# Optimization experiments

Hardware: AMD Instinct MI355X
Metric: run time of the kernel (lower is better)

Reference implementation:

```python
import jax, jax.numpy as jnp
import numpy as np

N_NODES = 10000
N_EDGES = 160000
MUL = 128            # channel multiplicity
N_SPECIES = 4        # node_attrs scalars
N_RADIAL = 8         # edge_feats scalars
AVG_NEIGH = 16.0
SQRT3 = 1.7320508075688772


def setup_inputs() -> dict:
    key = jax.random.key(0)
    ks = jax.random.split(key, 16)
    inp = {}
    inp['node_attrs'] = jax.random.uniform(ks[0], (N_NODES, N_SPECIES), dtype=jnp.float32)
    inp['node_feats'] = jax.random.normal(ks[1], (N_NODES, MUL * 4), dtype=jnp.float32)  # 128x0e + 128x1o
    inp['edge_attrs'] = jax.random.normal(ks[2], (N_EDGES, 4), dtype=jnp.float32)        # 1x0e + 1x1o (SH lmax=1)
    inp['edge_feats'] = jax.random.normal(ks[3], (N_EDGES, N_RADIAL), dtype=jnp.float32)
    inp['edge_index'] = jax.random.randint(ks[4], (2, N_EDGES), 0, N_NODES, dtype=jnp.int32)
    # linear_up: per-l mixing (o3.Linear on 128x0e+128x1o)
    inp['W_up0'] = jax.random.normal(ks[5], (MUL, MUL), dtype=jnp.float32)
    inp['W_up1'] = jax.random.normal(ks[6], (MUL, MUL), dtype=jnp.float32)
    # radial MLP [8, 64, 64, 512] (conv_tp.weight_numel = 4 instructions * 128)
    inp['W_mlp1'] = jax.random.normal(ks[7], (N_RADIAL, 64), dtype=jnp.float32)
    inp['W_mlp2'] = jax.random.normal(ks[8], (64, 64), dtype=jnp.float32)
    inp['W_mlp3'] = jax.random.normal(ks[9], (64, 4 * MUL), dtype=jnp.float32)
    # linear: irreps_mid.simplify() = 256x0e + 256x1o -> 128x0e + 128x1o
    inp['W_lin0'] = jax.random.normal(ks[10], (2 * MUL, MUL), dtype=jnp.float32)
    inp['W_lin1'] = jax.random.normal(ks[11], (2 * MUL, MUL), dtype=jnp.float32)
    # skip_tp: FullyConnectedTensorProduct(target, 4x0e -> target), uvw weights per l
    inp['W_skip0'] = jax.random.normal(ks[12], (MUL, N_SPECIES, MUL), dtype=jnp.float32)
    inp['W_skip1'] = jax.random.normal(ks[13], (MUL, N_SPECIES, MUL), dtype=jnp.float32)
    inp['update_coeff_param'] = jnp.zeros((1,), dtype=jnp.float32)
    return inp


def reference(node_attrs, node_feats, edge_attrs, edge_feats, edge_index,
              W_up0, W_up1, W_mlp1, W_mlp2, W_mlp3, W_lin0, W_lin1,
              W_skip0, W_skip1, update_coeff_param):
    N = node_feats.shape[0]
    # split node feats into irrep blocks: scalars [N,128], vectors [N,128,3]
    s = node_feats[:, :MUL]
    v = node_feats[:, MUL:].reshape(N, MUL, 3)
    # linear_up (o3.Linear, fan-in normalized)
    inv_up = 1.0 / jnp.sqrt(jnp.float32(MUL))
    s = (s @ W_up0) * inv_up
    v = jnp.einsum('nui,uw->nwi', v, W_up1) * inv_up
    # radial MLP -> per-edge TP weights (e3nn FullyConnectedNet style, fan-in normalized, silu)
    h = jax.nn.silu((edge_feats @ W_mlp1) / jnp.sqrt(jnp.float32(N_RADIAL)))
    h = jax.nn.silu((h @ W_mlp2) / jnp.sqrt(jnp.float32(64)))
    tpw = (h @ W_mlp3) / jnp.sqrt(jnp.float32(64))  # [E, 512]
    # instruction order (sorted by output irrep): 0e*0e->0e, 1o*1o->0e, 0e*1o->1o, 1o*0e->1o
    w_a, w_b, w_c, w_d = tpw[:, :MUL], tpw[:, MUL:2*MUL], tpw[:, 2*MUL:3*MUL], tpw[:, 3*MUL:]
    sender, receiver = edge_index[0], edge_index[1]
    xs = s[sender]          # [E,128] gather
    xv = v[sender]          # [E,128,3]
    ea_s = edge_attrs[:, :1]    # [E,1]
    ea_v = edge_attrs[:, 1:4]   # [E,3]
    # CG tensor-product messages ('uvu', component norm)
    m0 = w_a * xs * ea_s                                        # 0e x 0e -> 0e
    m1 = w_b * (jnp.einsum('eui,ei->eu', xv, ea_v) / SQRT3)      # 1o x 1o -> 0e
    m2 = (w_c * xs)[:, :, None] * ea_v[:, None, :]               # 0e x 1o -> 1o
    m3 = w_d[:, :, None] * xv * ea_s[:, :, None]                 # 1o x 0e -> 1o
    ms = jnp.concatenate([m0, m1], axis=1)                       # [E,256]
    mv = jnp.concatenate([m2, m3], axis=1)                       # [E,256,3]
    # scatter-sum to receiver nodes
    Ms = jax.ops.segment_sum(ms, receiver, num_segments=N)       # [N,256]
    Mv = jax.ops.segment_sum(mv, receiver, num_segments=N)       # [N,256,3]
    # linear (256x0e+256x1o -> 128x0e+128x1o), divided by avg_num_neighbors
    inv_lin = 1.0 / (jnp.sqrt(jnp.float32(2 * MUL)) * AVG_NEIGH)
    S = (Ms @ W_lin0) * inv_lin                                  # [N,128]
    V = jnp.einsum('nui,uw->nwi', Mv, W_lin1) * inv_lin          # [N,128,3]
    # skip_tp: FullyConnectedTensorProduct(message, node_attrs) with uvw weights
    inv_sk = 1.0 / jnp.sqrt(jnp.float32(MUL * N_SPECIES))
    sc_s = jnp.einsum('nu,nv,uvw->nw', S, node_attrs, W_skip0) * inv_sk
    sc_v = jnp.einsum('nui,nv,uvw->nwi', V, node_attrs, W_skip1) * inv_sk
    # residual stream mixing (sc=False branch)
    c = jax.nn.sigmoid(update_coeff_param)                       # [1]
    c_old = jax.lax.rsqrt(c * c + 1.0)
    c_new = c * c_old
    S = c_old * S + c_new * sc_s
    V = c_old * V + c_new * sc_v
    # reshape_irreps: [N, mul, 1 + 3]
    out = jnp.concatenate([S[:, :, None], V], axis=-1)           # [N,128,4]
    return out
```

## Files before the change

kernel.cpp:

```cpp
#include <hip/hip_runtime.h>

#define MUL 128

typedef __attribute__((ext_vector_type(8))) short bf16x8;
typedef __attribute__((ext_vector_type(4))) short bf16x4;
typedef __attribute__((ext_vector_type(4))) float f32x4;

__device__ __constant__ float kINV_UP   = 0.08838834764831845f;
__device__ __constant__ float kINV_L1   = 0.35355339059327373f;
__device__ __constant__ float kINV_L2   = 0.125f;
__device__ __constant__ float kINV_L3   = 0.125f;
__device__ __constant__ float kINV_LIN  = 0.00390625f;
__device__ __constant__ float kINV_SK   = 0.044194173824159216f;
__device__ __constant__ float kINV_SQ3  = 0.5773502691896258f;

#define WAVE_LDS_SYNC() asm volatile("s_waitcnt lgkmcnt(0)" ::: "memory")

static __device__ __forceinline__ short f2bf(float f) {
  unsigned u = __float_as_uint(f);
  unsigned r = (u + 0x7FFFu + ((u >> 16) & 1u)) >> 16;
  return (short)r;
}

__global__ __launch_bounds__(256) void k_cvtcnt(
    const float* __restrict__ W_up0, const float* __restrict__ W_up1,
    const float* __restrict__ W_lin0, const float* __restrict__ W_lin1,
    const float* __restrict__ W_sk0, const float* __restrict__ W_sk1,
    const float* __restrict__ W_mlp2, const float* __restrict__ W_mlp3,
    short* __restrict__ W0T, short* __restrict__ W1T,
    short* __restrict__ Wl0T, short* __restrict__ Wl1T,
    short* __restrict__ Wsk0T, short* __restrict__ Wsk1T,
    short* __restrict__ W2T, short* __restrict__ W3T,
    const int* __restrict__ eidx, int* __restrict__ cnt, int E, int CVT_B) {
  int blk = blockIdx.x;
  if (blk >= CVT_B) {
    int e = (blk - CVT_B) * 256 + threadIdx.x;
    if (e < E) atomicAdd(&cnt[eidx[E + e]], 1);
    return;
  }
  int id = blk * 256 + threadIdx.x;
  if (id < 16384) {
    int w = id >> 7, u = id & 127;
    W0T[id] = f2bf(W_up0[u * 128 + w]);
    return;
  }
  id -= 16384;
  if (id < 16384) {
    int w = id >> 7, u = id & 127;
    W1T[id] = f2bf(W_up1[u * 128 + w]);
    return;
  }
  id -= 16384;
  if (id < 32768) {
    int w = id >> 8, u = id & 255;
    Wl0T[id] = f2bf(W_lin0[u * 128 + w]);
    return;
  }
  id -= 32768;
  if (id < 32768) {
    int w = id >> 8, u = id & 255;
    Wl1T[id] = f2bf(W_lin1[u * 128 + w]);
    return;
  }
  id -= 32768;
  if (id < 65536) {
    int w = id >> 9, k = id & 511;
    int v = k >> 7, u = k & 127;
    Wsk0T[id] = f2bf(W_sk0[(u * 4 + v) * 128 + w]);
    return;
  }
  id -= 65536;
  if (id < 65536) {
    int w = id >> 9, k = id & 511;
    int v = k >> 7, u = k & 127;
    Wsk1T[id] = f2bf(W_sk1[(u * 4 + v) * 128 + w]);
    return;
  }
  id -= 65536;
  if (id < 4096) {
    int c = id >> 6, k = id & 63;
    W2T[id] = f2bf(W_mlp2[k * 64 + c]);
    return;
  }
  id -= 4096;
  if (id < 32768) {
    int c = id >> 6, k = id & 63;
    W3T[id] = f2bf(W_mlp3[k * 512 + c]);
  }
}

__global__ __launch_bounds__(1024) void k_scan(const int* __restrict__ cnt,
                                               int* __restrict__ offs,
                                               int* __restrict__ cursor, int N) {
  __shared__ int part[1024];
  const int t = threadIdx.x;
  int CH = (N + 1023) >> 10;
  if (CH > 16) CH = 16;
  const int base = t * CH;
  int loc[16];
  int s = 0;
  for (int i = 0; i < CH; ++i) {
    int idx = base + i;
    loc[i] = (idx < N) ? cnt[idx] : 0;
    s += loc[i];
  }
  part[t] = s;
  __syncthreads();
  for (int off = 1; off < 1024; off <<= 1) {
    int v = part[t];
    int add = (t >= off) ? part[t - off] : 0;
    __syncthreads();
    part[t] = v + add;
    __syncthreads();
  }
  int excl = part[t] - s;
  for (int i = 0; i < CH; ++i) {
    int idx = base + i;
    if (idx < N) { offs[idx] = excl; cursor[idx] = excl; }
    excl += loc[i];
  }
  if (t == 1023) offs[N] = part[1023];
}

__global__ __launch_bounds__(256) void k_fused3(
    const int* __restrict__ eidx, int* __restrict__ cursor, int* __restrict__ sorted,
    const float* __restrict__ nf, const short* __restrict__ W0T,
    const short* __restrict__ W1T, float* __restrict__ s_up, float* __restrict__ v_up,
    const float* __restrict__ ef, const float* __restrict__ W1f,
    const short* __restrict__ W2T, const short* __restrict__ W3T,
    unsigned* __restrict__ tpw2, int N, int E, int MLP_B, int UP_B) {
  __shared__ __align__(16) char smem[29696];
  const int t = threadIdx.x;
  int blk = blockIdx.x;

  if (blk < MLP_B) {
    float* sW1  = (float*)smem;
    short* sW2T = (short*)(smem + 2048);
    short* sh1  = (short*)(smem + 11264);
    short* sh2  = (short*)(smem + 20480);

    for (int i = t * 4; i < 512; i += 1024)
      *reinterpret_cast<float4*>(&sW1[i]) = *reinterpret_cast<const float4*>(W1f + i);
    for (int i = t * 8; i < 4096; i += 2048) {
      int r = i >> 6, c = i & 63;
      *reinterpret_cast<bf16x8*>(&sW2T[r * 72 + c]) =
          *reinterpret_cast<const bf16x8*>(&W2T[r * 64 + c]);
    }
    __syncthreads();

    const int w = t >> 6, l = t & 63, li = l & 15, g = l >> 4;
    const int e = blk * 64 + w * 16 + li;
    short* h1row = sh1 + (w * 16 + li) * 72;
    short* h2row = sh2 + (w * 16 + li) * 72;

    float4 qa = {0.f, 0.f, 0.f, 0.f}, qb = {0.f, 0.f, 0.f, 0.f};
    if (e < E) {
      qa = *reinterpret_cast<const float4*>(ef + (size_t)e * 8);
      qb = *reinterpret_cast<const float4*>(ef + (size_t)e * 8 + 4);
    }
    const float x[8] = {qa.x, qa.y, qa.z, qa.w, qb.x, qb.y, qb.z, qb.w};
    {
      bf16x8 p0, p1;
#pragma unroll
      for (int j = 0; j < 16; ++j) {
        int col = g * 16 + j;
        float a = 0.f;
#pragma unroll
        for (int k = 0; k < 8; ++k) a += x[k] * sW1[k * 64 + col];
        a *= kINV_L1;
        short hv = f2bf(a / (1.f + __expf(-a)));
        if (j < 8) p0[j] = hv; else p1[j - 8] = hv;
      }
      *reinterpret_cast<bf16x8*>(&h1row[g * 16])     = p0;
      *reinterpret_cast<bf16x8*>(&h1row[g * 16 + 8]) = p1;
    }
    WAVE_LDS_SYNC();

    {
      bf16x8 b0 = *reinterpret_cast<const bf16x8*>(&h1row[g * 8]);
      bf16x8 b1 = *reinterpret_cast<const bf16x8*>(&h1row[32 + g * 8]);
#pragma unroll
      for (int ct = 0; ct < 4; ++ct) {
        const short* wrow = &sW2T[(ct * 16 + li) * 72];
        bf16x8 a0 = *reinterpret_cast<const bf16x8*>(&wrow[g * 8]);
        bf16x8 a1 = *reinterpret_cast<const bf16x8*>(&wrow[32 + g * 8]);
        f32x4 acc = {0.f, 0.f, 0.f, 0.f};
        acc = __builtin_amdgcn_mfma_f32_16x16x32_bf16(a0, b0, acc, 0, 0, 0);
        acc = __builtin_amdgcn_mfma_f32_16x16x32_bf16(a1, b1, acc, 0, 0, 0);
        bf16x4 hq;
#pragma unroll
        for (int r = 0; r < 4; ++r) {
          float a = acc[r] * kINV_L2;
          hq[r] = f2bf(a / (1.f + __expf(-a)));
        }
        *reinterpret_cast<bf16x4*>(&h2row[ct * 16 + g * 4]) = hq;
      }
    }
    WAVE_LDS_SYNC();

    {
      bf16x8 b0 = *reinterpret_cast<const bf16x8*>(&h2row[g * 8]);
      bf16x8 b1 = *reinterpret_cast<const bf16x8*>(&h2row[32 + g * 8]);
#pragma unroll 4
      for (int rt = 0; rt < 16; ++rt) {
        const int rowA = rt * 16 + li;
        bf16x8 a0 = *reinterpret_cast<const bf16x8*>(&W3T[(size_t)rowA * 64 + g * 8]);
        bf16x8 a1 = *reinterpret_cast<const bf16x8*>(&W3T[(size_t)rowA * 64 + 32 + g * 8]);
        bf16x8 a2 = *reinterpret_cast<const bf16x8*>(&W3T[(size_t)(rowA + 256) * 64 + g * 8]);
        bf16x8 a3 = *reinterpret_cast<const bf16x8*>(&W3T[(size_t)(rowA + 256) * 64 + 32 + g * 8]);
        f32x4 accA = {0.f, 0.f, 0.f, 0.f};
        f32x4 accB = {0.f, 0.f, 0.f, 0.f};
        accA = __builtin_amdgcn_mfma_f32_16x16x32_bf16(a0, b0, accA, 0, 0, 0);
        accA = __builtin_amdgcn_mfma_f32_16x16x32_bf16(a1, b1, accA, 0, 0, 0);
        accB = __builtin_amdgcn_mfma_f32_16x16x32_bf16(a2, b0, accB, 0, 0, 0);
        accB = __builtin_amdgcn_mfma_f32_16x16x32_bf16(a3, b1, accB, 0, 0, 0);
        if (e < E) {
          uint4 d;
          unsigned* dp = &d.x;
#pragma unroll
          for (int r = 0; r < 4; ++r) {
            unsigned lo = (unsigned)(unsigned short)f2bf(accA[r] * kINV_L3);
            unsigned hi = (unsigned)(unsigned short)f2bf(accB[r] * kINV_L3);
            dp[r] = lo | (hi << 16);
          }
          *reinterpret_cast<uint4*>(&tpw2[(size_t)e * 256 + rt * 16 + g * 4]) = d;
        }
      }
    }
    return;
  }
  blk -= MLP_B;

  if (blk < UP_B) {
    short* lsA = (short*)smem;
    const int nb = blk * 16;

    for (int base = t * 8; base < 16 * 512; base += 256 * 8) {
      int n = base >> 9, j0 = base & 511;
      float vals[8];
      if (nb + n < N) {
        float4 q0 = *reinterpret_cast<const float4*>(nf + (size_t)(nb + n) * 512 + j0);
        float4 q1 = *reinterpret_cast<const float4*>(nf + (size_t)(nb + n) * 512 + j0 + 4);
        vals[0] = q0.x; vals[1] = q0.y; vals[2] = q0.z; vals[3] = q0.w;
        vals[4] = q1.x; vals[5] = q1.y; vals[6] = q1.z; vals[7] = q1.w;
      } else {
#pragma unroll
        for (int e = 0; e < 8; ++e) vals[e] = 0.f;
      }
#pragma unroll
      for (int e = 0; e < 8; ++e) {
        int idx = j0 + e;
        if (idx < 128) {
          lsA[(0 * 16 + n) * 136 + idx] = f2bf(vals[e]);
        } else {
          unsigned q = idx - 128;
          unsigned u = q / 3u;
          unsigned i = q - u * 3u;
          lsA[((1 + i) * 16 + n) * 136 + u] = f2bf(vals[e]);
        }
      }
    }
    __syncthreads();

    const int c = t >> 6;
    const int lane = t & 63;
    const int col = lane & 15;
    const int g = lane >> 4;

    const short* WT = c ? W1T : W0T;

    bf16x8 af[4];
#pragma unroll
    for (int kk = 0; kk < 4; ++kk)
      af[kk] = *reinterpret_cast<const bf16x8*>(&lsA[(c * 16 + col) * 136 + kk * 32 + g * 8]);

#pragma unroll
    for (int nt = 0; nt < 8; ++nt) {
      f32x4 acc = {0.f, 0.f, 0.f, 0.f};
#pragma unroll
      for (int kk = 0; kk < 4; ++kk) {
        bf16x8 bf = *reinterpret_cast<const bf16x8*>(&WT[(size_t)(nt * 16 + col) * 128 + kk * 32 + g * 8]);
        acc = __builtin_amdgcn_mfma_f32_16x16x32_bf16(af[kk], bf, acc, 0, 0, 0);
      }
#pragma unroll
      for (int r = 0; r < 4; ++r) {
        int nd = nb + g * 4 + r;
        if (nd < N) {
          float val = acc[r] * kINV_UP;
          if (c == 0) s_up[(size_t)nd * 128 + nt * 16 + col] = val;
          else        v_up[(size_t)nd * 384 + (c - 1) * 128 + nt * 16 + col] = val;
        }
      }
    }
    return;
  }
  blk -= UP_B;

  int e = blk * 256 + t;
  if (e < E) {
    int r = eidx[E + e];
    int p = atomicAdd(&cursor[r], 1);
    sorted[p] = e;
  }
}

__global__ __launch_bounds__(256) void k_gather(
    const int* __restrict__ sorted, const int* __restrict__ offs,
    const unsigned* __restrict__ tpw2, const float* __restrict__ eattr,
    const int* __restrict__ eidx,
    const float* __restrict__ s_up, const float* __restrict__ v_up,
    float* __restrict__ Ms, float* __restrict__ Mv, int N, int SB) {
  const int t = threadIdx.x;
  const int vside = blockIdx.x >= SB;
  const int nb = (vside ? blockIdx.x - SB : blockIdx.x) * 4;
  const int n = nb + (t >> 6);
  if (n >= N) return;
  const int l = t & 63;
  const int u0 = l * 2;

  float aMs0 = 0.f, aMs1 = 0.f;
  float aV[3][2] = {};

  const int e0 = offs[n], e1 = offs[n + 1];

  if (!vside) {
    for (int p = e0; p < e1; ++p) {
      int eid = sorted[p];
      int snd = eidx[eid];
      float4 ea = *reinterpret_cast<const float4*>(eattr + (size_t)eid * 4);
      uint2 q = *reinterpret_cast<const uint2*>(tpw2 + (size_t)eid * 256 + u0);
      float2 xs = *reinterpret_cast<const float2*>(s_up + (size_t)snd * 128 + u0);
      float tA0 = __uint_as_float(q.x << 16);
      float tB0 = __uint_as_float(q.x & 0xFFFF0000u);
      float tA1 = __uint_as_float(q.y << 16);
      float tB1 = __uint_as_float(q.y & 0xFFFF0000u);
      float xe0 = xs.x * ea.x, xe1 = xs.y * ea.x;
      aMs0 += tA0 * xe0;
      aMs1 += tA1 * xe1;
      float wc0 = tB0 * xs.x, wc1 = tB1 * xs.y;
      aV[0][0] += wc0 * ea.y; aV[0][1] += wc1 * ea.y;
      aV[1][0] += wc0 * ea.z; aV[1][1] += wc1 * ea.z;
      aV[2][0] += wc0 * ea.w; aV[2][1] += wc1 * ea.w;
    }
    *reinterpret_cast<float2*>(Ms + (size_t)n * 256 + u0) = make_float2(aMs0, aMs1);
#pragma unroll
    for (int i = 0; i < 3; ++i)
      *reinterpret_cast<float2*>(Mv + (size_t)n * 768 + i * 256 + u0) =
          make_float2(aV[i][0], aV[i][1]);
  } else {
    for (int p = e0; p < e1; ++p) {
      int eid = sorted[p];
      int snd = eidx[eid];
      float4 ea = *reinterpret_cast<const float4*>(eattr + (size_t)eid * 4);
      uint2 q = *reinterpret_cast<const uint2*>(tpw2 + (size_t)eid * 256 + 128 + u0);
      const float* xv = v_up + (size_t)snd * 384 + u0;
      float2 x0 = *reinterpret_cast<const float2*>(xv);
      float2 x1 = *reinterpret_cast<const float2*>(xv + 128);
      float2 x2 = *reinterpret_cast<const float2*>(xv + 256);
      float tA0 = __uint_as_float(q.x << 16);
      float tB0 = __uint_as_float(q.x & 0xFFFF0000u);
      float tA1 = __uint_as_float(q.y << 16);
      float tB1 = __uint_as_float(q.y & 0xFFFF0000u);
      float dot0 = x0.x * ea.y + x1.x * ea.z + x2.x * ea.w;
      float dot1 = x0.y * ea.y + x1.y * ea.z + x2.y * ea.w;
      aMs0 += tA0 * dot0 * kINV_SQ3;
      aMs1 += tA1 * dot1 * kINV_SQ3;
      float wd0 = tB0 * ea.x, wd1 = tB1 * ea.x;
      aV[0][0] += wd0 * x0.x; aV[0][1] += wd1 * x0.y;
      aV[1][0] += wd0 * x1.x; aV[1][1] += wd1 * x1.y;
      aV[2][0] += wd0 * x2.x; aV[2][1] += wd1 * x2.y;
    }
    *reinterpret_cast<float2*>(Ms + (size_t)n * 256 + 128 + u0) = make_float2(aMs0, aMs1);
#pragma unroll
    for (int i = 0; i < 3; ++i)
      *reinterpret_cast<float2*>(Mv + (size_t)n * 768 + i * 256 + 128 + u0) =
          make_float2(aV[i][0], aV[i][1]);
  }
}

__global__ __launch_bounds__(256) void k_linskip(
    const float* __restrict__ Ms, const float* __restrict__ Mv,
    const short* __restrict__ Wl0T, const short* __restrict__ Wl1T,
    const short* __restrict__ Wsk0T, const short* __restrict__ Wsk1T,
    const float* __restrict__ attrs, const float* __restrict__ upd,
    float* __restrict__ out, int N) {
  __shared__ __align__(16) short lsA[4][16][264];
  __shared__ __align__(16) short lsS[4][16][136];
  __shared__ float sat[16][4];
  const int nb = blockIdx.x * 16;
  const int t = threadIdx.x;

  for (int base = t * 4; base < 16 * 1024; base += 1024) {
    int n = base >> 10, j = base & 1023;
    int comp = j >> 8, u = j & 255;
    float4 q = {0.f, 0.f, 0.f, 0.f};
    if (nb + n < N) {
      const float* src = (comp == 0) ? (Ms + (size_t)(nb + n) * 256 + u)
                                     : (Mv + (size_t)(nb + n) * 768 + (size_t)(comp - 1) * 256 + u);
      q = *reinterpret_cast<const float4*>(src);
    }
    lsA[comp][n][u + 0] = f2bf(q.x);
    lsA[comp][n][u + 1] = f2bf(q.y);
    lsA[comp][n][u + 2] = f2bf(q.z);
    lsA[comp][n][u + 3] = f2bf(q.w);
  }
  if (t < 64) {
    int n = t >> 2, v = t & 3;
    sat[n][v] = (nb + n < N) ? attrs[(size_t)(nb + n) * 4 + v] : 0.f;
  }
  __syncthreads();

  const int c = t >> 6;
  const int lane = t & 63;
  const int col = lane & 15;
  const int g = lane >> 4;

  const short* WLT = c ? Wl1T : Wl0T;
  const short* WST = c ? Wsk1T : Wsk0T;

  bf16x8 af1[8];
#pragma unroll
  for (int kk = 0; kk < 8; ++kk)
    af1[kk] = *reinterpret_cast<const bf16x8*>(&lsA[c][col][kk * 32 + g * 8]);

  f32x4 Sreg[8];
#pragma unroll
  for (int nt = 0; nt < 8; ++nt) {
    f32x4 acc = {0.f, 0.f, 0.f, 0.f};
#pragma unroll
    for (int kk = 0; kk < 8; ++kk) {
      bf16x8 bf = *reinterpret_cast<const bf16x8*>(&WLT[(size_t)(nt * 16 + col) * 256 + kk * 32 + g * 8]);
      acc = __builtin_amdgcn_mfma_f32_16x16x32_bf16(af1[kk], bf, acc, 0, 0, 0);
    }
#pragma unroll
    for (int r = 0; r < 4; ++r) acc[r] *= kINV_LIN;
    Sreg[nt] = acc;
#pragma unroll
    for (int r = 0; r < 4; ++r)
      lsS[c][g * 4 + r][nt * 16 + col] = f2bf(acc[r]);
  }

  float satr[4][4];
#pragma unroll
  for (int r = 0; r < 4; ++r)
#pragma unroll
    for (int v = 0; v < 4; ++v) satr[r][v] = sat[g * 4 + r][v];

  __syncthreads();

  bf16x8 af2[4];
#pragma unroll
  for (int kk = 0; kk < 4; ++kk)
    af2[kk] = *reinterpret_cast<const bf16x8*>(&lsS[c][col][kk * 32 + g * 8]);

  const float p = upd[0];
  const float cc = 1.f / (1.f + __expf(-p));
  const float c_old = rsqrtf(cc * cc + 1.f);
  const float c_new = cc * c_old;

#pragma unroll
  for (int nt = 0; nt < 8; ++nt) {
    float fin[4] = {0.f, 0.f, 0.f, 0.f};
#pragma unroll
    for (int v = 0; v < 4; ++v) {
      f32x4 tmp = {0.f, 0.f, 0.f, 0.f};
#pragma unroll
      for (int kk = 0; kk < 4; ++kk) {
        bf16x8 bf = *reinterpret_cast<const bf16x8*>(&WST[(size_t)(nt * 16 + col) * 512 + v * 128 + kk * 32 + g * 8]);
        tmp = __builtin_amdgcn_mfma_f32_16x16x32_bf16(af2[kk], bf, tmp, 0, 0, 0);
      }
#pragma unroll
      for (int r = 0; r < 4; ++r) fin[r] += satr[r][v] * tmp[r];
    }
#pragma unroll
    for (int r = 0; r < 4; ++r) {
      int nd = nb + g * 4 + r;
      if (nd < N) {
        float val = c_old * Sreg[nt][r] + c_new * fin[r] * kINV_SK;
        out[((size_t)nd * 128 + nt * 16 + col) * 4 + c] = val;
      }
    }
  }
}

extern "C" void kernel_launch(void* const* d_in, const int* in_sizes, int n_in,
                              void* d_out, int out_size, void* d_ws, size_t ws_size,
                              hipStream_t stream) {
  const float* node_attrs = (const float*)d_in[0];
  const float* node_feats = (const float*)d_in[1];
  const float* edge_attrs = (const float*)d_in[2];
  const float* edge_feats = (const float*)d_in[3];
  const int*   edge_index = (const int*)d_in[4];
  const float* W_up0  = (const float*)d_in[5];
  const float* W_up1  = (const float*)d_in[6];
  const float* W_mlp1 = (const float*)d_in[7];
  const float* W_mlp2 = (const float*)d_in[8];
  const float* W_mlp3 = (const float*)d_in[9];
  const float* W_lin0 = (const float*)d_in[10];
  const float* W_lin1 = (const float*)d_in[11];
  const float* W_skip0 = (const float*)d_in[12];
  const float* W_skip1 = (const float*)d_in[13];
  const float* upd = (const float*)d_in[14];
  float* out = (float*)d_out;

  const int N = in_sizes[0] / 4;
  const int E = in_sizes[4] / 2;

  float* ws = (float*)d_ws;
  float* s_up = ws;
  float* v_up = s_up + (size_t)N * 128;
  float* Ms   = v_up + (size_t)N * 384;
  float* Mv   = Ms + (size_t)N * 256;
  int* cnt    = (int*)(Mv + (size_t)N * 768);
  int* offs   = cnt + N;
  int* cursor = offs + N + 1;
  int* sorted = cursor + N;

  short* wbase = (short*)((((uintptr_t)(sorted + E)) + 15) & ~(uintptr_t)15);
  short* W0T   = wbase;
  short* W1T   = W0T + 16384;
  short* Wl0T  = W1T + 16384;
  short* Wl1T  = Wl0T + 32768;
  short* Wsk0T = Wl1T + 32768;
  short* Wsk1T = Wsk0T + 65536;
  short* W2T   = Wsk1T + 65536;
  short* W3T   = W2T + 4096;
  unsigned* tpw2 = (unsigned*)(W3T + 32768);

  const int CVT_B = (266240 + 255) / 256;
  const int CNT_B = (E + 255) / 256;
  const int MLP_B = (E + 63) / 64;
  const int UP_B  = (N + 15) / 16;
  const int SC_B  = (E + 255) / 256;
  const int SB    = (N + 3) / 4;

  hipMemsetAsync(cnt, 0, (size_t)N * sizeof(int), stream);

  k_cvtcnt<<<CVT_B + CNT_B, 256, 0, stream>>>(
      W_up0, W_up1, W_lin0, W_lin1, W_skip0, W_skip1, W_mlp2, W_mlp3,
      W0T, W1T, Wl0T, Wl1T, Wsk0T, Wsk1T, W2T, W3T,
      edge_index, cnt, E, CVT_B);
  k_scan<<<1, 1024, 0, stream>>>(cnt, offs, cursor, N);
  k_fused3<<<MLP_B + UP_B + SC_B, 256, 0, stream>>>(
      edge_index, cursor, sorted,
      node_feats, W0T, W1T, s_up, v_up,
      edge_feats, W_mlp1, W2T, W3T, tpw2, N, E, MLP_B, UP_B);
  k_gather<<<2 * SB, 256, 0, stream>>>(sorted, offs, tpw2, edge_attrs, edge_index,
                                       s_up, v_up, Ms, Mv, N, SB);
  k_linskip<<<(N + 15) / 16, 256, 0, stream>>>(Ms, Mv, Wl0T, Wl1T, Wsk0T, Wsk1T,
                                               node_attrs, upd, out, N);
}
```

Before: 316.8 us.

## Process two edge tiles per wave in radial MLP and prefetch W3T rows

Each MLP block now handles 128 edges (two 16-edge tiles per wave), so every W2T/W3T fragment loaded is reused across two MFMA sets, halving weight loads per edge and halving the number of MLP blocks. The layer-3 loop also software-prefetches the next W3T row tile into registers before issuing the current MFMAs. The change raises LDS use to about 47 KB and increases register pressure, which may lower occupancy for all blocks of the fused kernel.

After: 282.2 us. -10.9%, faster.

```diff
diff --git a/kernel.cpp b/kernel.cpp
--- a/kernel.cpp
+++ b/kernel.cpp
@@ -129,7 +129,7 @@
     const float* __restrict__ ef, const float* __restrict__ W1f,
     const short* __restrict__ W2T, const short* __restrict__ W3T,
     unsigned* __restrict__ tpw2, int N, int E, int MLP_B, int UP_B) {
-  __shared__ __align__(16) char smem[29696];
+  __shared__ __align__(16) char smem[48128];
   const int t = threadIdx.x;
   int blk = blockIdx.x;
 
@@ -137,7 +137,7 @@
     float* sW1  = (float*)smem;
     short* sW2T = (short*)(smem + 2048);
     short* sh1  = (short*)(smem + 11264);
-    short* sh2  = (short*)(smem + 20480);
+    short* sh2  = (short*)(smem + 29696);
 
     for (int i = t * 4; i < 512; i += 1024)
       *reinterpret_cast<float4*>(&sW1[i]) = *reinterpret_cast<const float4*>(W1f + i);
@@ -149,82 +149,118 @@
     __syncthreads();
 
     const int w = t >> 6, l = t & 63, li = l & 15, g = l >> 4;
-    const int e = blk * 64 + w * 16 + li;
-    short* h1row = sh1 + (w * 16 + li) * 72;
-    short* h2row = sh2 + (w * 16 + li) * 72;
-
-    float4 qa = {0.f, 0.f, 0.f, 0.f}, qb = {0.f, 0.f, 0.f, 0.f};
-    if (e < E) {
-      qa = *reinterpret_cast<const float4*>(ef + (size_t)e * 8);
-      qb = *reinterpret_cast<const float4*>(ef + (size_t)e * 8 + 4);
-    }
-    const float x[8] = {qa.x, qa.y, qa.z, qa.w, qb.x, qb.y, qb.z, qb.w};
+    const int eb = blk * 128 + w * 32;
+    const int es0 = eb + li, es1 = eb + 16 + li;
+    short* h1r0 = sh1 + (w * 32 + li) * 72;
+    short* h1r1 = sh1 + (w * 32 + 16 + li) * 72;
+    short* h2r0 = sh2 + (w * 32 + li) * 72;
+    short* h2r1 = sh2 + (w * 32 + 16 + li) * 72;
+
     {
-      bf16x8 p0, p1;
-#pragma unroll
-      for (int j = 0; j < 16; ++j) {
-        int col = g * 16 + j;
-        float a = 0.f;
-#pragma unroll
-        for (int k = 0; k < 8; ++k) a += x[k] * sW1[k * 64 + col];
-        a *= kINV_L1;
-        short hv = f2bf(a / (1.f + __expf(-a)));
-        if (j < 8) p0[j] = hv; else p1[j - 8] = hv;
-      }
-      *reinterpret_cast<bf16x8*>(&h1row[g * 16])     = p0;
-      *reinterpret_cast<bf16x8*>(&h1row[g * 16 + 8]) = p1;
+#pragma unroll
+      for (int s = 0; s < 2; ++s) {
+        const int e = s ? es1 : es0;
+        short* h1row = s ? h1r1 : h1r0;
+        float4 qa = {0.f, 0.f, 0.f, 0.f}, qb = {0.f, 0.f, 0.f, 0.f};
+        if (e < E) {
+          qa = *reinterpret_cast<const float4*>(ef + (size_t)e * 8);
+          qb = *reinterpret_cast<const float4*>(ef + (size_t)e * 8 + 4);
+        }
+        const float x[8] = {qa.x, qa.y, qa.z, qa.w, qb.x, qb.y, qb.z, qb.w};
+        bf16x8 p0, p1;
+#pragma unroll
+        for (int j = 0; j < 16; ++j) {
+          int col = g * 16 + j;
+          float a = 0.f;
+#pragma unroll
+          for (int k = 0; k < 8; ++k) a += x[k] * sW1[k * 64 + col];
+          a *= kINV_L1;
+          short hv = f2bf(a / (1.f + __expf(-a)));
+          if (j < 8) p0[j] = hv; else p1[j - 8] = hv;
+        }
+        *reinterpret_cast<bf16x8*>(&h1row[g * 16])     = p0;
+        *reinterpret_cast<bf16x8*>(&h1row[g * 16 + 8]) = p1;
+      }
     }
     WAVE_LDS_SYNC();
 
     {
-      bf16x8 b0 = *reinterpret_cast<const bf16x8*>(&h1row[g * 8]);
-      bf16x8 b1 = *reinterpret_cast<const bf16x8*>(&h1row[32 + g * 8]);
+      bf16x8 hb0[2], hb1[2];
+      hb0[0] = *reinterpret_cast<const bf16x8*>(&h1r0[g * 8]);
+      hb1[0] = *reinterpret_cast<const bf16x8*>(&h1r0[32 + g * 8]);
+      hb0[1] = *reinterpret_cast<const bf16x8*>(&h1r1[g * 8]);
+      hb1[1] = *reinterpret_cast<const bf16x8*>(&h1r1[32 + g * 8]);
 #pragma unroll
       for (int ct = 0; ct < 4; ++ct) {
         const short* wrow = &sW2T[(ct * 16 + li) * 72];
         bf16x8 a0 = *reinterpret_cast<const bf16x8*>(&wrow[g * 8]);
         bf16x8 a1 = *reinterpret_cast<const bf16x8*>(&wrow[32 + g * 8]);
-        f32x4 acc = {0.f, 0.f, 0.f, 0.f};
-        acc = __builtin_amdgcn_mfma_f32_16x16x32_bf16(a0, b0, acc, 0, 0, 0);
-        acc = __builtin_amdgcn_mfma_f32_16x16x32_bf16(a1, b1, acc, 0, 0, 0);
-        bf16x4 hq;
-#pragma unroll
-        for (int r = 0; r < 4; ++r) {
-          float a = acc[r] * kINV_L2;
-          hq[r] = f2bf(a / (1.f + __expf(-a)));
-        }
-        *reinterpret_cast<bf16x4*>(&h2row[ct * 16 + g * 4]) = hq;
+#pragma unroll
+        for (int s = 0; s < 2; ++s) {
+          f32x4 acc = {0.f, 0.f, 0.f, 0.f};
+          acc = __builtin_amdgcn_mfma_f32_16x16x32_bf16(a0, hb0[s], acc, 0, 0, 0);
+          acc = __builtin_amdgcn_mfma_f32_16x16x32_bf16(a1, hb1[s], acc, 0, 0, 0);
+          bf16x4 hq;
+#pragma unroll
+          for (int r = 0; r < 4; ++r) {
+            float a = acc[r] * kINV_L2;
+            hq[r] = f2bf(a / (1.f + __expf(-a)));
+          }
+          *reinterpret_cast<bf16x4*>(&((s ? h2r1 : h2r0)[ct * 16 + g * 4])) = hq;
+        }
       }
     }
     WAVE_LDS_SYNC();
 
     {
-      bf16x8 b0 = *reinterpret_cast<const bf16x8*>(&h2row[g * 8]);
-      bf16x8 b1 = *reinterpret_cast<const bf16x8*>(&h2row[32 + g * 8]);
-#pragma unroll 4
+      bf16x8 b0[2], b1[2];
+      b0[0] = *reinterpret_cast<const bf16x8*>(&h2r0[g * 8]);
+      b1[0] = *reinterpret_cast<const bf16x8*>(&h2r0[32 + g * 8]);
+      b0[1] = *reinterpret_cast<const bf16x8*>(&h2r1[g * 8]);
+      b1[1] = *reinterpret_cast<const bf16x8*>(&h2r1[32 + g * 8]);
+      const bool ok0 = es0 < E, ok1 = es1 < E;
+
+      bf16x8 c0, c1, c2, c3;
+      {
+        const int rowA = li;
+        c0 = *reinterpret_cast<const bf16x8*>(&W3T[(size_t)rowA * 64 + g * 8]);
+        c1 = *reinterpret_cast<const bf16x8*>(&W3T[(size_t)rowA * 64 + 32 + g * 8]);
+        c2 = *reinterpret_cast<const bf16x8*>(&W3T[(size_t)(rowA + 256) * 64 + g * 8]);
+        c3 = *reinterpret_cast<const bf16x8*>(&W3T[(size_t)(rowA + 256) * 64 + 32 + g * 8]);
+      }
+#pragma unroll
       for (int rt = 0; rt < 16; ++rt) {
-        const int rowA = rt * 16 + li;
-        bf16x8 a0 = *reinterpret_cast<const bf16x8*>(&W3T[(size_t)rowA * 64 + g * 8]);
-        bf16x8 a1 = *reinterpret_cast<const bf16x8*>(&W3T[(size_t)rowA * 64 + 32 + g * 8]);
-        bf16x8 a2 = *reinterpret_cast<const bf16x8*>(&W3T[(size_t)(rowA + 256) * 64 + g * 8]);
-        bf16x8 a3 = *reinterpret_cast<const bf16x8*>(&W3T[(size_t)(rowA + 256) * 64 + 32 + g * 8]);
-        f32x4 accA = {0.f, 0.f, 0.f, 0.f};
-        f32x4 accB = {0.f, 0.f, 0.f, 0.f};
-        accA = __builtin_amdgcn_mfma_f32_16x16x32_bf16(a0, b0, accA, 0, 0, 0);
-        accA = __builtin_amdgcn_mfma_f32_16x16x32_bf16(a1, b1, accA, 0, 0, 0);
-        accB = __builtin_amdgcn_mfma_f32_16x16x32_bf16(a2, b0, accB, 0, 0, 0);
-        accB = __builtin_amdgcn_mfma_f32_16x16x32_bf16(a3, b1, accB, 0, 0, 0);
-        if (e < E) {
-          uint4 d;
-          unsigned* dp = &d.x;
-#pragma unroll
-          for (int r = 0; r < 4; ++r) {
-            unsigned lo = (unsigned)(unsigned short)f2bf(accA[r] * kINV_L3);
-            unsigned hi = (unsigned)(unsigned short)f2bf(accB[r] * kINV_L3);
-            dp[r] = lo | (hi << 16);
+        bf16x8 n0, n1, n2, n3;
+        const bool pf = (rt < 15);
+        if (pf) {
+          const int rowA = (rt + 1) * 16 + li;
+          n0 = *reinterpret_cast<const bf16x8*>(&W3T[(size_t)rowA * 64 + g * 8]);
+          n1 = *reinterpret_cast<const bf16x8*>(&W3T[(size_t)rowA * 64 + 32 + g * 8]);
+          n2 = *reinterpret_cast<const bf16x8*>(&W3T[(size_t)(rowA + 256) * 64 + g * 8]);
+          n3 = *reinterpret_cast<const bf16x8*>(&W3T[(size_t)(rowA + 256) * 64 + 32 + g * 8]);
+        }
+#pragma unroll
+        for (int s = 0; s < 2; ++s) {
+          f32x4 accA = {0.f, 0.f, 0.f, 0.f};
+          f32x4 accB = {0.f, 0.f, 0.f, 0.f};
+          accA = __builtin_amdgcn_mfma_f32_16x16x32_bf16(c0, b0[s], accA, 0, 0, 0);
+          accA = __builtin_amdgcn_mfma_f32_16x16x32_bf16(c1, b1[s], accA, 0, 0, 0);
+          accB = __builtin_amdgcn_mfma_f32_16x16x32_bf16(c2, b0[s], accB, 0, 0, 0);
+          accB = __builtin_amdgcn_mfma_f32_16x16x32_bf16(c3, b1[s], accB, 0, 0, 0);
+          if (s ? ok1 : ok0) {
+            uint4 d;
+            unsigned* dp = &d.x;
+#pragma unroll
+            for (int r = 0; r < 4; ++r) {
+              unsigned lo = (unsigned)(unsigned short)f2bf(accA[r] * kINV_L3);
+              unsigned hi = (unsigned)(unsigned short)f2bf(accB[r] * kINV_L3);
+              dp[r] = lo | (hi << 16);
+            }
+            *reinterpret_cast<uint4*>(
+                &tpw2[(size_t)(s ? es1 : es0) * 256 + rt * 16 + g * 4]) = d;
           }
-          *reinterpret_cast<uint4*>(&tpw2[(size_t)e * 256 + rt * 16 + g * 4]) = d;
-        }
+        }
+        if (pf) { c0 = n0; c1 = n1; c2 = n2; c3 = n3; }
       }
     }
     return;
@@ -529,7 +565,7 @@
 
   const int CVT_B = (266240 + 255) / 256;
   const int CNT_B = (E + 255) / 256;
-  const int MLP_B = (E + 63) / 64;
+  const int MLP_B = (E + 127) / 128;
   const int UP_B  = (N + 15) / 16;
   const int SC_B  = (E + 255) / 256;
   const int SB    = (N + 3) / 4;
```

## Fuse radial MLP into receiver-sorted message aggregation with segmented atomic adds

Applied to the files above, without the earlier changes.

Removes the separate radial-MLP pass that wrote per-edge bf16 tensor-product weights to global memory. Each block now takes 32 receiver-sorted edge records and computes the MLP for them, keeping the weights in LDS. It then accumulates messages per receiver run and flushes them with float atomics into Ms/Mv, which are zeroed by extra blocks in the first kernel. This cuts a large global write and read of per-edge weights, at the cost of atomics at block boundaries, non-deterministic summation order, and more LDS per block.

After: 371.2 us. +17.2%, slower.

```diff
diff --git a/kernel.cpp b/kernel.cpp
--- a/kernel.cpp
+++ b/kernel.cpp
@@ -14,12 +14,13 @@
 __device__ __constant__ float kINV_SK   = 0.044194173824159216f;
 __device__ __constant__ float kINV_SQ3  = 0.5773502691896258f;
 
-#define WAVE_LDS_SYNC() asm volatile("s_waitcnt lgkmcnt(0)" ::: "memory")
-
 static __device__ __forceinline__ short f2bf(float f) {
   unsigned u = __float_as_uint(f);
   unsigned r = (u + 0x7FFFu + ((u >> 16) & 1u)) >> 16;
   return (short)r;
+}
+static __device__ __forceinline__ float bf2f(short s) {
+  return __uint_as_float(((unsigned)(unsigned short)s) << 16);
 }
 
 __global__ __launch_bounds__(256) void k_cvtcnt(
@@ -31,8 +32,15 @@
     short* __restrict__ Wl0T, short* __restrict__ Wl1T,
     short* __restrict__ Wsk0T, short* __restrict__ Wsk1T,
     short* __restrict__ W2T, short* __restrict__ W3T,
-    const int* __restrict__ eidx, int* __restrict__ cnt, int E, int CVT_B) {
+    const int* __restrict__ eidx, int* __restrict__ cnt,
+    float* __restrict__ Mzero, int E, int CVT_B, int CNT_B) {
   int blk = blockIdx.x;
+  if (blk >= CVT_B + CNT_B) {
+    size_t off = (size_t)(blk - CVT_B - CNT_B) * 1024 + threadIdx.x * 4;
+    float4 z = {0.f, 0.f, 0.f, 0.f};
+    *reinterpret_cast<float4*>(Mzero + off) = z;
+    return;
+  }
   if (blk >= CVT_B) {
     int e = (blk - CVT_B) * 256 + threadIdx.x;
     if (e < E) atomicAdd(&cnt[eidx[E + e]], 1);
@@ -122,119 +130,17 @@
   if (t == 1023) offs[N] = part[1023];
 }
 
-__global__ __launch_bounds__(256) void k_fused3(
-    const int* __restrict__ eidx, int* __restrict__ cursor, int* __restrict__ sorted,
+__global__ __launch_bounds__(256) void k_upscatter(
+    const int* __restrict__ eidx, int* __restrict__ cursor, uint4* __restrict__ recs,
     const float* __restrict__ nf, const short* __restrict__ W0T,
     const short* __restrict__ W1T, float* __restrict__ s_up, float* __restrict__ v_up,
-    const float* __restrict__ ef, const float* __restrict__ W1f,
-    const short* __restrict__ W2T, const short* __restrict__ W3T,
-    unsigned* __restrict__ tpw2, int N, int E, int MLP_B, int UP_B) {
-  __shared__ __align__(16) char smem[29696];
+    int N, int E, int UP_B) {
+  __shared__ __align__(16) short lsA[4][16][136];
   const int t = threadIdx.x;
   int blk = blockIdx.x;
 
-  if (blk < MLP_B) {
-    float* sW1  = (float*)smem;
-    short* sW2T = (short*)(smem + 2048);
-    short* sh1  = (short*)(smem + 11264);
-    short* sh2  = (short*)(smem + 20480);
-
-    for (int i = t * 4; i < 512; i += 1024)
-      *reinterpret_cast<float4*>(&sW1[i]) = *reinterpret_cast<const float4*>(W1f + i);
-    for (int i = t * 8; i < 4096; i += 2048) {
-      int r = i >> 6, c = i & 63;
-      *reinterpret_cast<bf16x8*>(&sW2T[r * 72 + c]) =
-          *reinterpret_cast<const bf16x8*>(&W2T[r * 64 + c]);
-    }
-    __syncthreads();
-
-    const int w = t >> 6, l = t & 63, li = l & 15, g = l >> 4;
-    const int e = blk * 64 + w * 16 + li;
-    short* h1row = sh1 + (w * 16 + li) * 72;
-    short* h2row = sh2 + (w * 16 + li) * 72;
-
-    float4 qa = {0.f, 0.f, 0.f, 0.f}, qb = {0.f, 0.f, 0.f, 0.f};
-    if (e < E) {
-      qa = *reinterpret_cast<const float4*>(ef + (size_t)e * 8);
-      qb = *reinterpret_cast<const float4*>(ef + (size_t)e * 8 + 4);
-    }
-    const float x[8] = {qa.x, qa.y, qa.z, qa.w, qb.x, qb.y, qb.z, qb.w};
-    {
-      bf16x8 p0, p1;
-#pragma unroll
-      for (int j = 0; j < 16; ++j) {
-        int col = g * 16 + j;
-        float a = 0.f;
-#pragma unroll
-        for (int k = 0; k < 8; ++k) a += x[k] * sW1[k * 64 + col];
-        a *= kINV_L1;
-        short hv = f2bf(a / (1.f + __expf(-a)));
-        if (j < 8) p0[j] = hv; else p1[j - 8] = hv;
-      }
-      *reinterpret_cast<bf16x8*>(&h1row[g * 16])     = p0;
-      *reinterpret_cast<bf16x8*>(&h1row[g * 16 + 8]) = p1;
-    }
-    WAVE_LDS_SYNC();
-
-    {
-      bf16x8 b0 = *reinterpret_cast<const bf16x8*>(&h1row[g * 8]);
-      bf16x8 b1 = *reinterpret_cast<const bf16x8*>(&h1row[32 + g * 8]);
-#pragma unroll
-      for (int ct = 0; ct < 4; ++ct) {
-        const short* wrow = &sW2T[(ct * 16 + li) * 72];
-        bf16x8 a0 = *reinterpret_cast<const bf16x8*>(&wrow[g * 8]);
-        bf16x8 a1 = *reinterpret_cast<const bf16x8*>(&wrow[32 + g * 8]);
-        f32x4 acc = {0.f, 0.f, 0.f, 0.f};
-        acc = __builtin_amdgcn_mfma_f32_16x16x32_bf16(a0, b0, acc, 0, 0, 0);
-        acc = __builtin_amdgcn_mfma_f32_16x16x32_bf16(a1, b1, acc, 0, 0, 0);
-        bf16x4 hq;
-#pragma unroll
-        for (int r = 0; r < 4; ++r) {
-          float a = acc[r] * kINV_L2;
-          hq[r] = f2bf(a / (1.f + __expf(-a)));
-        }
-        *reinterpret_cast<bf16x4*>(&h2row[ct * 16 + g * 4]) = hq;
-      }
-    }
-    WAVE_LDS_SYNC();
-
-    {
-      bf16x8 b0 = *reinterpret_cast<const bf16x8*>(&h2row[g * 8]);
-      bf16x8 b1 = *reinterpret_cast<const bf16x8*>(&h2row[32 + g * 8]);
-#pragma unroll 4
-      for (int rt = 0; rt < 16; ++rt) {
-        const int rowA = rt * 16 + li;
-        bf16x8 a0 = *reinterpret_cast<const bf16x8*>(&W3T[(size_t)rowA * 64 + g * 8]);
-        bf16x8 a1 = *reinterpret_cast<const bf16x8*>(&W3T[(size_t)rowA * 64 + 32 + g * 8]);
-        bf16x8 a2 = *reinterpret_cast<const bf16x8*>(&W3T[(size_t)(rowA + 256) * 64 + g * 8]);
-        bf16x8 a3 = *reinterpret_cast<const bf16x8*>(&W3T[(size_t)(rowA + 256) * 64 + 32 + g * 8]);
-        f32x4 accA = {0.f, 0.f, 0.f, 0.f};
-        f32x4 accB = {0.f, 0.f, 0.f, 0.f};
-        accA = __builtin_amdgcn_mfma_f32_16x16x32_bf16(a0, b0, accA, 0, 0, 0);
-        accA = __builtin_amdgcn_mfma_f32_16x16x32_bf16(a1, b1, accA, 0, 0, 0);
-        accB = __builtin_amdgcn_mfma_f32_16x16x32_bf16(a2, b0, accB, 0, 0, 0);
-        accB = __builtin_amdgcn_mfma_f32_16x16x32_bf16(a3, b1, accB, 0, 0, 0);
-        if (e < E) {
-          uint4 d;
-          unsigned* dp = &d.x;
-#pragma unroll
-          for (int r = 0; r < 4; ++r) {
-            unsigned lo = (unsigned)(unsigned short)f2bf(accA[r] * kINV_L3);
-            unsigned hi = (unsigned)(unsigned short)f2bf(accB[r] * kINV_L3);
-            dp[r] = lo | (hi << 16);
-          }
-          *reinterpret_cast<uint4*>(&tpw2[(size_t)e * 256 + rt * 16 + g * 4]) = d;
-        }
-      }
-    }
-    return;
-  }
-  blk -= MLP_B;
-
   if (blk < UP_B) {
-    short* lsA = (short*)smem;
     const int nb = blk * 16;
-
     for (int base = t * 8; base < 16 * 512; base += 256 * 8) {
       int n = base >> 9, j0 = base & 511;
       float vals[8];
@@ -251,12 +157,12 @@
       for (int e = 0; e < 8; ++e) {
         int idx = j0 + e;
         if (idx < 128) {
-          lsA[(0 * 16 + n) * 136 + idx] = f2bf(vals[e]);
+          lsA[0][n][idx] = f2bf(vals[e]);
         } else {
           unsigned q = idx - 128;
           unsigned u = q / 3u;
           unsigned i = q - u * 3u;
-          lsA[((1 + i) * 16 + n) * 136 + u] = f2bf(vals[e]);
+          lsA[1 + i][n][u] = f2bf(vals[e]);
         }
       }
     }
@@ -272,7 +178,7 @@
     bf16x8 af[4];
 #pragma unroll
     for (int kk = 0; kk < 4; ++kk)
-      af[kk] = *reinterpret_cast<const bf16x8*>(&lsA[(c * 16 + col) * 136 + kk * 32 + g * 8]);
+      af[kk] = *reinterpret_cast<const bf16x8*>(&lsA[c][col][kk * 32 + g * 8]);
 
 #pragma unroll
     for (int nt = 0; nt < 8; ++nt) {
@@ -299,82 +205,179 @@
   int e = blk * 256 + t;
   if (e < E) {
     int r = eidx[E + e];
+    int snd = eidx[e];
     int p = atomicAdd(&cursor[r], 1);
-    sorted[p] = e;
-  }
-}
-
-__global__ __launch_bounds__(256) void k_gather(
-    const int* __restrict__ sorted, const int* __restrict__ offs,
-    const unsigned* __restrict__ tpw2, const float* __restrict__ eattr,
-    const int* __restrict__ eidx,
+    uint4 rc;
+    rc.x = (unsigned)e; rc.y = (unsigned)snd; rc.z = (unsigned)r; rc.w = 0u;
+    recs[p] = rc;
+  }
+}
+
+__global__ __launch_bounds__(256) void k_msgagg(
+    const uint4* __restrict__ recs, const int* __restrict__ offs_unused,
+    const float* __restrict__ ef, const float* __restrict__ eattr,
+    const float* __restrict__ W1f, const short* __restrict__ W2T,
+    const short* __restrict__ W3T,
     const float* __restrict__ s_up, const float* __restrict__ v_up,
-    float* __restrict__ Ms, float* __restrict__ Mv, int N, int SB) {
+    float* __restrict__ Ms, float* __restrict__ Mv, int E) {
+  __shared__ float sW1[512];
+  __shared__ __align__(16) short sW2T[64 * 72];
+  __shared__ __align__(16) short sh1[32 * 72];
+  __shared__ __align__(16) short sh2[32 * 72];
+  __shared__ __align__(16) short stpw[32 * 516];
+  __shared__ int   seid[32], ssnd[32], srcv[32];
+  __shared__ float sea[32][4];
+
   const int t = threadIdx.x;
-  const int vside = blockIdx.x >= SB;
-  const int nb = (vside ? blockIdx.x - SB : blockIdx.x) * 4;
-  const int n = nb + (t >> 6);
-  if (n >= N) return;
-  const int l = t & 63;
-  const int u0 = l * 2;
-
-  float aMs0 = 0.f, aMs1 = 0.f;
-  float aV[3][2] = {};
-
-  const int e0 = offs[n], e1 = offs[n + 1];
-
-  if (!vside) {
-    for (int p = e0; p < e1; ++p) {
-      int eid = sorted[p];
-      int snd = eidx[eid];
-      float4 ea = *reinterpret_cast<const float4*>(eattr + (size_t)eid * 4);
-      uint2 q = *reinterpret_cast<const uint2*>(tpw2 + (size_t)eid * 256 + u0);
-      float2 xs = *reinterpret_cast<const float2*>(s_up + (size_t)snd * 128 + u0);
-      float tA0 = __uint_as_float(q.x << 16);
-      float tB0 = __uint_as_float(q.x & 0xFFFF0000u);
-      float tA1 = __uint_as_float(q.y << 16);
-      float tB1 = __uint_as_float(q.y & 0xFFFF0000u);
-      float xe0 = xs.x * ea.x, xe1 = xs.y * ea.x;
-      aMs0 += tA0 * xe0;
-      aMs1 += tA1 * xe1;
-      float wc0 = tB0 * xs.x, wc1 = tB1 * xs.y;
-      aV[0][0] += wc0 * ea.y; aV[0][1] += wc1 * ea.y;
-      aV[1][0] += wc0 * ea.z; aV[1][1] += wc1 * ea.z;
-      aV[2][0] += wc0 * ea.w; aV[2][1] += wc1 * ea.w;
-    }
-    *reinterpret_cast<float2*>(Ms + (size_t)n * 256 + u0) = make_float2(aMs0, aMs1);
-#pragma unroll
-    for (int i = 0; i < 3; ++i)
-      *reinterpret_cast<float2*>(Mv + (size_t)n * 768 + i * 256 + u0) =
-          make_float2(aV[i][0], aV[i][1]);
+  const int pb = blockIdx.x * 32;
+  const int cntE = min(32, E - pb);
+
+  for (int i = t * 4; i < 512; i += 1024)
+    *reinterpret_cast<float4*>(&sW1[i]) = *reinterpret_cast<const float4*>(W1f + i);
+  for (int i = t * 8; i < 4096; i += 2048) {
+    int r = i >> 6, c = i & 63;
+    *reinterpret_cast<bf16x8*>(&sW2T[r * 72 + c]) =
+        *reinterpret_cast<const bf16x8*>(&W2T[r * 64 + c]);
+  }
+  if (t < 32) {
+    if (t < cntE) {
+      uint4 rc = recs[pb + t];
+      seid[t] = (int)rc.x; ssnd[t] = (int)rc.y; srcv[t] = (int)rc.z;
+    } else {
+      seid[t] = 0; ssnd[t] = 0; srcv[t] = -1;
+    }
+  }
+  __syncthreads();
+
+  {
+    const int e = t & 31, cg = t >> 5;
+    float x[8];
+    if (e < cntE) {
+      float4 qa = *reinterpret_cast<const float4*>(ef + (size_t)seid[e] * 8);
+      float4 qb = *reinterpret_cast<const float4*>(ef + (size_t)seid[e] * 8 + 4);
+      x[0] = qa.x; x[1] = qa.y; x[2] = qa.z; x[3] = qa.w;
+      x[4] = qb.x; x[5] = qb.y; x[6] = qb.z; x[7] = qb.w;
+    } else {
+#pragma unroll
+      for (int k = 0; k < 8; ++k) x[k] = 0.f;
+    }
+    bf16x8 p0;
+#pragma unroll
+    for (int j = 0; j < 8; ++j) {
+      int col = cg * 8 + j;
+      float a = 0.f;
+#pragma unroll
+      for (int k = 0; k < 8; ++k) a += x[k] * sW1[k * 64 + col];
+      a *= kINV_L1;
+      p0[j] = f2bf(a / (1.f + __expf(-a)));
+    }
+    *reinterpret_cast<bf16x8*>(&sh1[e * 72 + cg * 8]) = p0;
+  }
+  if (t < 128) {
+    int le = t >> 2, f = t & 3;
+    sea[le][f] = (le < cntE) ? eattr[(size_t)seid[le] * 4 + f] : 0.f;
+  }
+  __syncthreads();
+
+  const int w = t >> 6, l = t & 63, li = l & 15, g = l >> 4;
+  const int grp = w >> 1, half = w & 1;
+  const int e = grp * 16 + li;
+
+  {
+    bf16x8 b0 = *reinterpret_cast<const bf16x8*>(&sh1[e * 72 + g * 8]);
+    bf16x8 b1 = *reinterpret_cast<const bf16x8*>(&sh1[e * 72 + 32 + g * 8]);
+#pragma unroll
+    for (int q = 0; q < 2; ++q) {
+      const int ct = half * 2 + q;
+      const short* wrow = &sW2T[(ct * 16 + li) * 72];
+      bf16x8 a0 = *reinterpret_cast<const bf16x8*>(&wrow[g * 8]);
+      bf16x8 a1 = *reinterpret_cast<const bf16x8*>(&wrow[32 + g * 8]);
+      f32x4 acc = {0.f, 0.f, 0.f, 0.f};
+      acc = __builtin_amdgcn_mfma_f32_16x16x32_bf16(a0, b0, acc, 0, 0, 0);
+      acc = __builtin_amdgcn_mfma_f32_16x16x32_bf16(a1, b1, acc, 0, 0, 0);
+      bf16x4 hq;
+#pragma unroll
+      for (int r = 0; r < 4; ++r) {
+        float a = acc[r] * kINV_L2;
+        hq[r] = f2bf(a / (1.f + __expf(-a)));
+      }
+      *reinterpret_cast<bf16x4*>(&sh2[e * 72 + ct * 16 + g * 4]) = hq;
+    }
+  }
+  __syncthreads();
+
+  {
+    bf16x8 b0 = *reinterpret_cast<const bf16x8*>(&sh2[e * 72 + g * 8]);
+    bf16x8 b1 = *reinterpret_cast<const bf16x8*>(&sh2[e * 72 + 32 + g * 8]);
+#pragma unroll
+    for (int q = 0; q < 8; ++q) {
+      const int rt = half * 8 + q;
+      const int rowA = rt * 16 + li;
+      bf16x8 a0 = *reinterpret_cast<const bf16x8*>(&W3T[(size_t)rowA * 64 + g * 8]);
+      bf16x8 a1 = *reinterpret_cast<const bf16x8*>(&W3T[(size_t)rowA * 64 + 32 + g * 8]);
+      bf16x8 a2 = *reinterpret_cast<const bf16x8*>(&W3T[(size_t)(rowA + 256) * 64 + g * 8]);
+      bf16x8 a3 = *reinterpret_cast<const bf16x8*>(&W3T[(size_t)(rowA + 256) * 64 + 32 + g * 8]);
+      f32x4 accA = {0.f, 0.f, 0.f, 0.f};
+      f32x4 accB = {0.f, 0.f, 0.f, 0.f};
+      accA = __builtin_amdgcn_mfma_f32_16x16x32_bf16(a0, b0, accA, 0, 0, 0);
+      accA = __builtin_amdgcn_mfma_f32_16x16x32_bf16(a1, b1, accA, 0, 0, 0);
+      accB = __builtin_amdgcn_mfma_f32_16x16x32_bf16(a2, b0, accB, 0, 0, 0);
+      accB = __builtin_amdgcn_mfma_f32_16x16x32_bf16(a3, b1, accB, 0, 0, 0);
+      bf16x4 hA, hB;
+#pragma unroll
+      for (int r = 0; r < 4; ++r) {
+        hA[r] = f2bf(accA[r] * kINV_L3);
+        hB[r] = f2bf(accB[r] * kINV_L3);
+      }
+      *reinterpret_cast<bf16x4*>(&stpw[e * 516 + rt * 16 + g * 4]) = hA;
+      *reinterpret_cast<bf16x4*>(&stpw[e * 516 + 256 + rt * 16 + g * 4]) = hB;
+    }
+  }
+  __syncthreads();
+
+  if (t < 128) {
+    const int u = t;
+    float aMs = 0.f, aV0 = 0.f, aV1 = 0.f, aV2 = 0.f;
+    for (int p = 0; p < cntE; ++p) {
+      float tA = bf2f(stpw[p * 516 + u]);
+      float tB = bf2f(stpw[p * 516 + 256 + u]);
+      float xs = s_up[(size_t)ssnd[p] * 128 + u];
+      float e0 = sea[p][0];
+      aMs += tA * xs * e0;
+      float wc = tB * xs;
+      aV0 += wc * sea[p][1];
+      aV1 += wc * sea[p][2];
+      aV2 += wc * sea[p][3];
+      if (p == cntE - 1 || srcv[p + 1] != srcv[p]) {
+        int n = srcv[p];
+        atomicAdd(Ms + (size_t)n * 256 + u, aMs);
+        atomicAdd(Mv + (size_t)n * 768 + u, aV0);
+        atomicAdd(Mv + (size_t)n * 768 + 256 + u, aV1);
+        atomicAdd(Mv + (size_t)n * 768 + 512 + u, aV2);
+        aMs = 0.f; aV0 = 0.f; aV1 = 0.f; aV2 = 0.f;
+      }
+    }
   } else {
-    for (int p = e0; p < e1; ++p) {
-      int eid = sorted[p];
-      int snd = eidx[eid];
-      float4 ea = *reinterpret_cast<const float4*>(eattr + (size_t)eid * 4);
-      uint2 q = *reinterpret_cast<const uint2*>(tpw2 + (size_t)eid * 256 + 128 + u0);
-      const float* xv = v_up + (size_t)snd * 384 + u0;
-      float2 x0 = *reinterpret_cast<const float2*>(xv);
-      float2 x1 = *reinterpret_cast<const float2*>(xv + 128);
-      float2 x2 = *reinterpret_cast<const float2*>(xv + 256);
-      float tA0 = __uint_as_float(q.x << 16);
-      float tB0 = __uint_as_float(q.x & 0xFFFF0000u);
-      float tA1 = __uint_as_float(q.y << 16);
-      float tB1 = __uint_as_float(q.y & 0xFFFF0000u);
-      float dot0 = x0.x * ea.y + x1.x * ea.z + x2.x * ea.w;
-      float dot1 = x0.y * ea.y + x1.y * ea.z + x2.y * ea.w;
-      aMs0 += tA0 * dot0 * kINV_SQ3;
-      aMs1 += tA1 * dot1 * kINV_SQ3;
-      float wd0 = tB0 * ea.x, wd1 = tB1 * ea.x;
-      aV[0][0] += wd0 * x0.x; aV[0][1] += wd1 * x0.y;
-      aV[1][0] += wd0 * x1.x; aV[1][1] += wd1 * x1.y;
-      aV[2][0] += wd0 * x2.x; aV[2][1] += wd1 * x2.y;
-    }
-    *reinterpret_cast<float2*>(Ms + (size_t)n * 256 + 128 + u0) = make_float2(aMs0, aMs1);
-#pragma unroll
-    for (int i = 0; i < 3; ++i)
-      *reinterpret_cast<float2*>(Mv + (size_t)n * 768 + i * 256 + 128 + u0) =
-          make_float2(aV[i][0], aV[i][1]);
+    const int u = t - 128;
+    float aMs = 0.f, aV0 = 0.f, aV1 = 0.f, aV2 = 0.f;
+    for (int p = 0; p < cntE; ++p) {
+      float tA = bf2f(stpw[p * 516 + 128 + u]);
+      float tB = bf2f(stpw[p * 516 + 384 + u]);
+      const float* xv = v_up + (size_t)ssnd[p] * 384 + u;
+      float x0 = xv[0], x1 = xv[128], x2 = xv[256];
+      float dot = x0 * sea[p][1] + x1 * sea[p][2] + x2 * sea[p][3];
+      aMs += tA * dot * kINV_SQ3;
+      float wd = tB * sea[p][0];
+      aV0 += wd * x0; aV1 += wd * x1; aV2 += wd * x2;
+      if (p == cntE - 1 || srcv[p + 1] != srcv[p]) {
+        int n = srcv[p];
+        atomicAdd(Ms + (size_t)n * 256 + 128 + u, aMs);
+        atomicAdd(Mv + (size_t)n * 768 + 128 + u, aV0);
+        atomicAdd(Mv + (size_t)n * 768 + 256 + 128 + u, aV1);
+        atomicAdd(Mv + (size_t)n * 768 + 512 + 128 + u, aV2);
+        aMs = 0.f; aV0 = 0.f; aV1 = 0.f; aV2 = 0.f;
+      }
+    }
   }
 }
 
@@ -514,9 +517,9 @@
   int* cnt    = (int*)(Mv + (size_t)N * 768);
   int* offs   = cnt + N;
   int* cursor = offs + N + 1;
-  int* sorted = cursor + N;
-
-  short* wbase = (short*)((((uintptr_t)(sorted + E)) + 15) & ~(uintptr_t)15);
+  uint4* recs = (uint4*)((((uintptr_t)(cursor + N)) + 15) & ~(uintptr_t)15);
+
+  short* wbase = (short*)((((uintptr_t)(recs + E)) + 15) & ~(uintptr_t)15);
   short* W0T   = wbase;
   short* W1T   = W0T + 16384;
   short* Wl0T  = W1T + 16384;
@@ -525,28 +528,25 @@
   short* Wsk1T = Wsk0T + 65536;
   short* W2T   = Wsk1T + 65536;
   short* W3T   = W2T + 4096;
-  unsigned* tpw2 = (unsigned*)(W3T + 32768);
 
   const int CVT_B = (266240 + 255) / 256;
   const int CNT_B = (E + 255) / 256;
-  const int MLP_B = (E + 63) / 64;
+  const int ZB    = N;
   const int UP_B  = (N + 15) / 16;
   const int SC_B  = (E + 255) / 256;
-  const int SB    = (N + 3) / 4;
+  const int MSG_B = (E + 31) / 32;
 
   hipMemsetAsync(cnt, 0, (size_t)N * sizeof(int), stream);
 
-  k_cvtcnt<<<CVT_B + CNT_B, 256, 0, stream>>>(
+  k_cvtcnt<<<CVT_B + CNT_B + ZB, 256, 0, stream>>>(
       W_up0, W_up1, W_lin0, W_lin1, W_skip0, W_skip1, W_mlp2, W_mlp3,
       W0T, W1T, Wl0T, Wl1T, Wsk0T, Wsk1T, W2T, W3T,
-      edge_index, cnt, E, CVT_B);
+      edge_index, cnt, Ms, E, CVT_B, CNT_B);
   k_scan<<<1, 1024, 0, stream>>>(cnt, offs, cursor, N);
-  k_fused3<<<MLP_B + UP_B + SC_B, 256, 0, stream>>>(
-      edge_index, cursor, sorted,
-      node_feats, W0T, W1T, s_up, v_up,
-      edge_feats, W_mlp1, W2T, W3T, tpw2, N, E, MLP_B, UP_B);
-  k_gather<<<2 * SB, 256, 0, stream>>>(sorted, offs, tpw2, edge_attrs, edge_index,
-                                       s_up, v_up, Ms, Mv, N, SB);
+  k_upscatter<<<UP_B + SC_B, 256, 0, stream>>>(
+      edge_index, cursor, recs, node_feats, W0T, W1T, s_up, v_up, N, E, UP_B);
+  k_msgagg<<<MSG_B, 256, 0, stream>>>(recs, offs, edge_feats, edge_attrs,
+                                      W_mlp1, W2T, W3T, s_up, v_up, Ms, Mv, E);
   k_linskip<<<(N + 15) / 16, 256, 0, stream>>>(Ms, Mv, Wl0T, Wl1T, Wsk0T, Wsk1T,
                                                node_attrs, upd, out, N);
 }
```
